# Performance work log

Hardware: AMD Instinct MI355X
Metric: run time of the kernel (lower is better)

## Reference

```python
import jax, jax.numpy as jnp
import numpy as np

N_DST = [50000, 10000, 2048]
HEADS = 4


def setup_inputs() -> dict:
    key = jax.random.key(0)
    ks = jax.random.split(key, 32)
    d = {}
    d["x"] = jax.random.normal(ks[0], (200000, 128), jnp.float32)
    # conv fc weights [in, H*D], attn vectors [H, D], bias [H*D]; skip [in, out]+bias
    conv_dims = [(128, 64), (256, 64), (256, 47)]   # (in, per-head out D)
    skip_dims = [(128, 256), (256, 256), (256, 47)]
    for l, ((cin, dph), (sin, sout)) in enumerate(zip(conv_dims, skip_dims)):
        d[f"W{l}"] = 0.1 * jax.random.normal(ks[1 + 5 * l], (cin, HEADS * dph), jnp.float32)
        d[f"al{l}"] = 0.1 * jax.random.normal(ks[2 + 5 * l], (HEADS, dph), jnp.float32)
        d[f"ar{l}"] = 0.1 * jax.random.normal(ks[3 + 5 * l], (HEADS, dph), jnp.float32)
        d[f"b{l}"] = jnp.zeros((HEADS * dph,), jnp.float32)
        d[f"Ws{l}"] = 0.1 * jax.random.normal(ks[4 + 5 * l], (sin, sout), jnp.float32)
        d[f"bs{l}"] = jnp.zeros((sout,), jnp.float32)
    edge_cfg = [(800000, 200000, 50000), (400000, 50000, 10000), (100000, 10000, 2048)]
    for l, (ne, ns, nd) in enumerate(edge_cfg):
        d[f"src{l}"] = jax.random.randint(ks[20 + 2 * l], (ne,), 0, ns, jnp.int32)
        d[f"dst{l}"] = jax.random.randint(ks[21 + 2 * l], (ne,), 0, nd, jnp.int32)
    return d


def gat_conv(h_src, h_dst, src, dst, n_dst, W, al, ar, b):
    H, D = al.shape
    fs = (h_src @ W).reshape(-1, H, D)   # [n_src, H, D]
    fd = (h_dst @ W).reshape(-1, H, D)   # [n_dst, H, D]
    el = jnp.einsum("nhd,hd->nh", fs, al)
    er = jnp.einsum("nhd,hd->nh", fd, ar)
    e = jax.nn.leaky_relu(el[src] + er[dst], 0.2)          # [E, H]
    emax = jax.ops.segment_max(e, dst, num_segments=n_dst)  # stable softmax
    ee = jnp.exp(e - emax[dst])
    denom = jax.ops.segment_sum(ee, dst, num_segments=n_dst)
    alpha = ee / denom[dst]
    msg = fs[src] * alpha[:, :, None]                      # [E, H, D]
    rst = jax.ops.segment_sum(msg, dst, num_segments=n_dst)
    return rst + b.reshape(1, H, D)


def reference(x, W0, al0, ar0, b0, Ws0, bs0, W1, al1, ar1, b1, Ws1, bs1,
              W2, al2, ar2, b2, Ws2, bs2, src0, dst0, src1, dst1, src2, dst2):
    h = x
    # layer 0
    h_res = h[:N_DST[0]]
    h = gat_conv(h, h_res, src0, dst0, N_DST[0], W0, al0, ar0, b0).reshape(N_DST[0], -1)
    h = jax.nn.elu(h + h_res @ Ws0 + bs0)
    # layer 1
    h_res = h[:N_DST[1]]
    h = gat_conv(h, h_res, src1, dst1, N_DST[1], W1, al1, ar1, b1).reshape(N_DST[1], -1)
    h = jax.nn.elu(h + h_res @ Ws1 + bs1)
    # layer 2: mean over heads, no activation
    h_res = h[:N_DST[2]]
    h = gat_conv(h, h_res, src2, dst2, N_DST[2], W2, al2, ar2, b2).mean(axis=1)
    h = h + h_res @ Ws2 + bs2
    return jax.nn.log_softmax(h, axis=-1)
```

## Files before the change

### kernel.cpp

```cpp
#include <hip/hip_runtime.h>
#include <hip/hip_bf16.h>
#include <cmath>

#define HEADS 4
typedef __hip_bfloat16 bf16;
typedef short short8 __attribute__((ext_vector_type(8)));
typedef unsigned short us8 __attribute__((ext_vector_type(8)));
typedef float floatx4 __attribute__((ext_vector_type(4)));
typedef float floatx2 __attribute__((ext_vector_type(2)));
typedef unsigned int u32;

__device__ inline float bf2f(unsigned short u) {
    union { unsigned u; float f; } c; c.u = ((unsigned)u) << 16; return c.f;
}
__device__ inline short f2bs(float f) {
    bf16 h = __float2bfloat16(f);
    return *reinterpret_cast<short*>(&h);
}
__device__ __forceinline__ floatx2 bfpair(unsigned u) {
    union { unsigned v; float f; } lo, hi;
    lo.v = u << 16; hi.v = u & 0xffff0000u;
    return (floatx2){lo.f, hi.f};
}
__device__ __forceinline__ unsigned char f2fp8(float v) {
    return (unsigned char)(__builtin_amdgcn_cvt_pk_fp8_f32(v, v, 0, false) & 0xff);
}

__device__ __forceinline__ void ld_lds16(const void* g, void* l) {
    __builtin_amdgcn_global_load_lds((const __attribute__((address_space(1))) u32*)g,
                                     (__attribute__((address_space(3))) u32*)l, 16, 0, 0);
}

__device__ const int g_ND[3]   = {50000, 10000, 2048};
__device__ const int g_OOFF[3] = {0, 50001, 60002};
__device__ const int g_NE[3]   = {800000, 400000, 100000};
__device__ const int g_SOFF[3] = {0, 800000, 1200000};
__device__ const int g_S[3]    = {391, 79, 16};

#define NBIN 128
#define NBLK 128
#define MAXB 8192
#define MAXS 391
#define PF 4

__global__ void precast_all(const float* __restrict__ W0, const float* __restrict__ W1,
                            const float* __restrict__ W2, const float* __restrict__ W3,
                            const float* __restrict__ W4, const float* __restrict__ x,
                            bf16* __restrict__ B0, bf16* __restrict__ B1, bf16* __restrict__ B2,
                            bf16* __restrict__ B3, bf16* __restrict__ B4, bf16* __restrict__ xb)
{
    int y = blockIdx.y;
    if (y == 5) {
        const float4* in = (const float4*)x;
        ushort4* out = (ushort4*)xb;
        const int n4 = 200000 * 128 / 4;
        for (int i = blockIdx.x * blockDim.x + threadIdx.x; i < n4; i += gridDim.x * blockDim.x) {
            float4 v = in[i];
            ushort4 o;
            o.x = (unsigned short)f2bs(v.x); o.y = (unsigned short)f2bs(v.y);
            o.z = (unsigned short)f2bs(v.z); o.w = (unsigned short)f2bs(v.w);
            out[i] = o;
        }
        return;
    }
    const int Ks[5] = {128, 256, 256, 128, 256};
    const int Ns[5] = {256, 256, 188, 256, 256};
    const float* W = (y == 0) ? W0 : (y == 1) ? W1 : (y == 2) ? W2 : (y == 3) ? W3 : W4;
    bf16* B = (y == 0) ? B0 : (y == 1) ? B1 : (y == 2) ? B2 : (y == 3) ? B3 : B4;
    int K = Ks[y], N = Ns[y], sz = K * N;
    for (int i = blockIdx.x * blockDim.x + threadIdx.x; i < sz; i += gridDim.x * blockDim.x) {
        int n = i / K, k = i % K;
        B[i] = __float2bfloat16(W[(size_t)k * N + n]);
    }
}

template<int FUSE, int EL, int OUT8>
__global__ __launch_bounds__(256)
void gemm_mfma(const bf16* __restrict__ A, const bf16* __restrict__ Bt,
               const bf16* __restrict__ add, const float* __restrict__ bias,
               const float* __restrict__ al, const float* __restrict__ ar,
               float* __restrict__ el, float* __restrict__ er,
               void* __restrict__ Cb, int M, int N, int K, int nd)
{
    const int BM = 128, BN = 128, BK = 64;
    __shared__ short As[BM * BK];
    __shared__ short Bs[BN * BK];
    int tid = threadIdx.x;
    int wave = tid >> 6, lane = tid & 63;
    int q = lane >> 4, r = lane & 15;
    int row0 = blockIdx.y * BM, col0 = blockIdx.x * BN;
    int wm = (wave >> 1) * 64, wn = (wave & 1) * 64;

    const short* A16 = (const short*)A;
    const short* B16 = (const short*)Bt;
    int srow = tid >> 3;
    int scol = ((tid & 7) ^ (srow & 7)) * 8;
    const short* ga = A16 + (size_t)(row0 + srow) * K + scol;
    const short* gb = B16 + (size_t)(col0 + srow) * K + scol;
    char* la = (char*)As + tid * 16;
    char* lb = (char*)Bs + tid * 16;

    floatx4 zero = {0.f, 0.f, 0.f, 0.f};
    floatx4 acc[4][4];
#pragma unroll
    for (int i = 0; i < 4; i++)
#pragma unroll
        for (int j = 0; j < 4; j++) acc[i][j] = zero;

    for (int k0 = 0; k0 < K; k0 += BK) {
        ld_lds16(ga,                    la);
        ld_lds16(ga + (size_t)32 * K,   la + 4096);
        ld_lds16(ga + (size_t)64 * K,   la + 8192);
        ld_lds16(ga + (size_t)96 * K,   la + 12288);
        ld_lds16(gb,                    lb);
        ld_lds16(gb + (size_t)32 * K,   lb + 4096);
        ld_lds16(gb + (size_t)64 * K,   lb + 8192);
        ld_lds16(gb + (size_t)96 * K,   lb + 12288);
        ga += BK; gb += BK;
        __syncthreads();
#pragma unroll
        for (int ks = 0; ks < 2; ks++) {
            short8 af[4], bfr[4];
#pragma unroll
            for (int mt = 0; mt < 4; mt++) {
                int row = wm + mt * 16 + r;
                af[mt] = *(short8*)&As[row * BK + (((ks << 2) | q) ^ (r & 7)) * 8];
            }
#pragma unroll
            for (int nt = 0; nt < 4; nt++) {
                int row = wn + nt * 16 + r;
                bfr[nt] = *(short8*)&Bs[row * BK + (((ks << 2) | q) ^ (r & 7)) * 8];
            }
#pragma unroll
            for (int mt = 0; mt < 4; mt++)
#pragma unroll
                for (int nt = 0; nt < 4; nt++)
                    acc[mt][nt] = __builtin_amdgcn_mfma_f32_16x16x32_bf16(af[mt], bfr[nt], acc[mt][nt], 0, 0, 0);
        }
        __syncthreads();
    }

#pragma unroll
    for (int mt = 0; mt < 4; mt++) {
#pragma unroll
        for (int nt = 0; nt < 4; nt++) {
            int gcol = col0 + wn + nt * 16 + r;
            if (gcol >= N) continue;
#pragma unroll
            for (int e = 0; e < 4; e++) {
                int grow = row0 + wm + mt * 16 + q * 4 + e;
                if (grow >= M) continue;
                float v = acc[mt][nt][e];
                size_t idx = (size_t)grow * N + gcol;
                if (FUSE == 1) {
                    v += __bfloat162float(add[idx]) + bias[gcol];
                    v = (v > 0.f) ? v : (__expf(v) - 1.f);
                }
                if (OUT8) ((unsigned char*)Cb)[idx] = f2fp8(v);
                else      ((bf16*)Cb)[idx] = __float2bfloat16(v);
            }
        }
    }

    if (EL) {
        int head = (col0 + wn) >> 6;
        float alh[4], arh[4];
#pragma unroll
        for (int nt = 0; nt < 4; nt++) {
            int c = nt * 16 + r;
            alh[nt] = al[head * 64 + c];
            arh[nt] = ar[head * 64 + c];
        }
#pragma unroll
        for (int mt = 0; mt < 4; mt++) {
#pragma unroll
            for (int e = 0; e < 4; e++) {
                float pl = 0.f, pr = 0.f;
#pragma unroll
                for (int nt = 0; nt < 4; nt++) {
                    float v = acc[mt][nt][e];
                    pl += v * alh[nt];
                    pr += v * arh[nt];
                }
#pragma unroll
                for (int off = 1; off < 16; off <<= 1) {
                    pl += __shfl_xor(pl, off);
                    pr += __shfl_xor(pr, off);
                }
                int grow = row0 + wm + mt * 16 + q * 4 + e;
                if (r == 0 && grow < M) {
                    el[grow * 4 + head] = pl;
                    if (grow < nd) er[grow * 4 + head] = pr;
                }
            }
        }
    }
}

__global__ void el_er_kernel(const bf16* __restrict__ fs, const float* __restrict__ al,
                             const float* __restrict__ ar, float* __restrict__ el,
                             float* __restrict__ er, int nd, int D)
{
    int n = blockIdx.x;
    int h = threadIdx.x >> 6;
    int d = threadIdx.x & 63;
    int HD = HEADS * D;
    float v = 0.f, a = 0.f, rr = 0.f;
    if (d < D) {
        v = __bfloat162float(fs[(size_t)n * HD + h * D + d]);
        a = al[h * D + d];
        rr = ar[h * D + d];
    }
    float pl = v * a, pr = v * rr;
    for (int off = 32; off; off >>= 1) {
        pl += __shfl_down(pl, off);
        pr += __shfl_down(pr, off);
    }
    if (d == 0) {
        el[n * HEADS + h] = pl;
        if (n < nd) er[n * HEADS + h] = pr;
    }
}

__global__ __launch_bounds__(256)
void bin_hist(const int* __restrict__ d0, const int* __restrict__ d1,
              const int* __restrict__ d2, int* __restrict__ blockhist)
{
    int l = blockIdx.y;
    const int* dst = (l == 0) ? d0 : (l == 1) ? d1 : d2;
    int ne = g_NE[l], S = g_S[l];
    __shared__ int h[NBIN];
    for (int i = threadIdx.x; i < NBIN; i += blockDim.x) h[i] = 0;
    __syncthreads();
    int per = (ne + NBLK - 1) / NBLK;
    int st = blockIdx.x * per;
    int en = min(st + per, ne);
    for (int i = st + threadIdx.x; i < en; i += blockDim.x)
        atomicAdd(&h[dst[i] / S], 1);
    __syncthreads();
    for (int i = threadIdx.x; i < NBIN; i += blockDim.x)
        blockhist[(l * NBIN + i) * NBLK + blockIdx.x] = h[i];
}

__global__ void coarse_scan(const int* __restrict__ blockhist, int* __restrict__ bbase,
                            int* __restrict__ offs)
{
    int l = blockIdx.x;
    int t = threadIdx.x;
    __shared__ int s[NBIN];
    int tot = 0;
    for (int k = 0; k < NBLK; k++) tot += blockhist[(l * NBIN + t) * NBLK + k];
    s[t] = tot;
    __syncthreads();
    for (int off = 1; off < NBIN; off <<= 1) {
        int a = (t >= off) ? s[t - off] : 0;
        __syncthreads();
        s[t] += a;
        __syncthreads();
    }
    bbase[l * (NBIN + 1) + t + 1] = s[t];
    if (t == 0) {
        bbase[l * (NBIN + 1)] = 0;
        offs[g_OOFF[l] + g_ND[l]] = g_NE[l];
    }
}

__global__ void bin_scan(const int* __restrict__ blockhist, const int* __restrict__ bbase,
                         int* __restrict__ base)
{
    int l = blockIdx.y, bin = blockIdx.x;
    int t = threadIdx.x;
    __shared__ int s[NBLK];
    int v = blockhist[(l * NBIN + bin) * NBLK + t];
    s[t] = v;
    __syncthreads();
    for (int off = 1; off < NBLK; off <<= 1) {
        int a = (t >= off) ? s[t - off] : 0;
        __syncthreads();
        s[t] += a;
        __syncthreads();
    }
    base[(l * NBIN + bin) * NBLK + t] = bbase[l * (NBIN + 1) + bin] + s[t] - v;
}

__global__ __launch_bounds__(256)
void bin_scatter(const int* __restrict__ s0, const int* __restrict__ d0,
                 const int* __restrict__ s1, const int* __restrict__ d1,
                 const int* __restrict__ s2, const int* __restrict__ d2,
                 const int* __restrict__ base, int* __restrict__ stage)
{
    int l = blockIdx.y;
    const int* src = (l == 0) ? s0 : (l == 1) ? s1 : s2;
    const int* dst = (l == 0) ? d0 : (l == 1) ? d1 : d2;
    int ne = g_NE[l], S = g_S[l], soff = g_SOFF[l];
    __shared__ int cur[NBIN];
    for (int i = threadIdx.x; i < NBIN; i += blockDim.x)
        cur[i] = base[(l * NBIN + i) * NBLK + blockIdx.x];
    __syncthreads();
    int per = (ne + NBLK - 1) / NBLK;
    int st = blockIdx.x * per;
    int en = min(st + per, ne);
    for (int i = st + threadIdx.x; i < en; i += blockDim.x) {
        int dv = dst[i];
        int b = dv / S;
        int ldst = dv - b * S;
        int p = atomicAdd(&cur[b], 1);
        stage[soff + p] = src[i] | (ldst << 18);
    }
}

__global__ __launch_bounds__(256)
void bin_expand(const int* __restrict__ stage, const int* __restrict__ bbase,
                int* __restrict__ offs, int* __restrict__ ssrc)
{
    int l = blockIdx.y, b = blockIdx.x;
    int S = g_S[l], nd = g_ND[l], ooff = g_OOFF[l], soff = g_SOFF[l];
    int dlo = b * S;
    if (dlo >= nd) return;
    int dhi = min(dlo + S, nd);
    int base = bbase[l * (NBIN + 1) + b];
    int end  = bbase[l * (NBIN + 1) + b + 1];
    int cnt  = end - base;
    int tid = threadIdx.x;
    __shared__ int sdata[MAXB];
    __shared__ int outb[MAXB];
    __shared__ int lh[512];
    __shared__ int lcur[MAXS];
    lh[tid] = 0; lh[tid + 256] = 0;
    __syncthreads();
    if (cnt <= MAXB) {
        for (int i = tid; i < cnt; i += 256) {
            int v = stage[soff + base + i];
            sdata[i] = v;
            atomicAdd(&lh[v >> 18], 1);
        }
        __syncthreads();
        for (int off = 1; off < 512; off <<= 1) {
            int a0 = (tid >= off) ? lh[tid - off] : 0;
            int a1 = lh[tid + 256 - off];
            __syncthreads();
            lh[tid] += a0; lh[tid + 256] += a1;
            __syncthreads();
        }
        for (int d = tid; d < dhi - dlo; d += 256) {
            int ex = (d == 0) ? 0 : lh[d - 1];
            offs[ooff + dlo + d] = base + ex;
            lcur[d] = ex;
        }
        __syncthreads();
        for (int i = tid; i < cnt; i += 256) {
            int v = sdata[i];
            int p = atomicAdd(&lcur[v >> 18], 1);
            outb[p] = v & 0x3FFFF;
        }
        __syncthreads();
        for (int i = tid; i < cnt; i += 256)
            ssrc[soff + base + i] = outb[i];
    } else {
        for (int i = tid; i < cnt; i += 256)
            atomicAdd(&lh[stage[soff + base + i] >> 18], 1);
        __syncthreads();
        for (int off = 1; off < 512; off <<= 1) {
            int a0 = (tid >= off) ? lh[tid - off] : 0;
            int a1 = lh[tid + 256 - off];
            __syncthreads();
            lh[tid] += a0; lh[tid + 256] += a1;
            __syncthreads();
        }
        for (int d = tid; d < dhi - dlo; d += 256) {
            int ex = (d == 0) ? 0 : lh[d - 1];
            offs[ooff + dlo + d] = base + ex;
            lcur[d] = ex;
        }
        __syncthreads();
        for (int i = tid; i < cnt; i += 256) {
            int v = stage[soff + base + i];
            int p = atomicAdd(&lcur[v >> 18], 1);
            ssrc[soff + base + p] = v & 0x3FFFF;
        }
    }
}

__global__ __launch_bounds__(256)
void attn_agg64(const unsigned char* __restrict__ fs8, const float* __restrict__ el,
                const float* __restrict__ er, const float* __restrict__ b,
                const int* __restrict__ offs, const int* __restrict__ ssrc,
                bf16* __restrict__ rst, int nd)
{
    int wave = threadIdx.x >> 6, lane = threadIdx.x & 63;
    int n = blockIdx.x * 4 + wave;
    if (n >= nd) return;
    int s0 = offs[n], s1 = offs[n + 1];
    float4 erv = *(const float4*)&er[(size_t)n * 4];
    int half = lane >> 5, sub = lane & 31, head = sub >> 3;
    float eh = (head == 0) ? erv.x : (head == 1) ? erv.y : (head == 2) ? erv.z : erv.w;

    floatx2 acc[4];
#pragma unroll
    for (int j = 0; j < 4; j++) acc[j] = (floatx2){0.f, 0.f};
    float s = 0.f;

    int cnt = s1 - s0;
    int npairs = cnt >> 1;
    int i = s0 + half;
    if (npairs > 0) {
        int sid = ssrc[i];
        float ev = el[(size_t)sid * 4 + head];
        uint2 f = *(const uint2*)&fs8[(size_t)sid * 256 + sub * 8];
        for (int p = 1; p < npairs; p++) {
            i += 2;
            int sid2 = ssrc[i];
            float ev2 = el[(size_t)sid2 * 4 + head];
            uint2 f2 = *(const uint2*)&fs8[(size_t)sid2 * 256 + sub * 8];
            float e = ev + eh; e = (e > 0.f) ? e : 0.2f * e;
            float a = __expf(fminf(e, 60.f));
            s += a;
            floatx2 aa = {a, a};
            acc[0] = __builtin_elementwise_fma((floatx2)__builtin_amdgcn_cvt_pk_f32_fp8(f.x, false), aa, acc[0]);
            acc[1] = __builtin_elementwise_fma((floatx2)__builtin_amdgcn_cvt_pk_f32_fp8(f.x, true),  aa, acc[1]);
            acc[2] = __builtin_elementwise_fma((floatx2)__builtin_amdgcn_cvt_pk_f32_fp8(f.y, false), aa, acc[2]);
            acc[3] = __builtin_elementwise_fma((floatx2)__builtin_amdgcn_cvt_pk_f32_fp8(f.y, true),  aa, acc[3]);
            ev = ev2; f = f2;
        }
        float e = ev + eh; e = (e > 0.f) ? e : 0.2f * e;
        float a = __expf(fminf(e, 60.f));
        s += a;
        floatx2 aa = {a, a};
        acc[0] = __builtin_elementwise_fma((floatx2)__builtin_amdgcn_cvt_pk_f32_fp8(f.x, false), aa, acc[0]);
        acc[1] = __builtin_elementwise_fma((floatx2)__builtin_amdgcn_cvt_pk_f32_fp8(f.x, true),  aa, acc[1]);
        acc[2] = __builtin_elementwise_fma((floatx2)__builtin_amdgcn_cvt_pk_f32_fp8(f.y, false), aa, acc[2]);
        acc[3] = __builtin_elementwise_fma((floatx2)__builtin_amdgcn_cvt_pk_f32_fp8(f.y, true),  aa, acc[3]);
    }
    if (cnt & 1) {
        int idx = s1 - 1;
        int sid = ssrc[idx];
        float ev = el[(size_t)sid * 4 + head];
        uint2 f = *(const uint2*)&fs8[(size_t)sid * 256 + sub * 8];
        float e = ev + eh; e = (e > 0.f) ? e : 0.2f * e;
        float a = __expf(fminf(e, 60.f));
        if (half) a = 0.f;
        s += a;
        floatx2 aa = {a, a};
        acc[0] = __builtin_elementwise_fma((floatx2)__builtin_amdgcn_cvt_pk_f32_fp8(f.x, false), aa, acc[0]);
        acc[1] = __builtin_elementwise_fma((floatx2)__builtin_amdgcn_cvt_pk_f32_fp8(f.x, true),  aa, acc[1]);
        acc[2] = __builtin_elementwise_fma((floatx2)__builtin_amdgcn_cvt_pk_f32_fp8(f.y, false), aa, acc[2]);
        acc[3] = __builtin_elementwise_fma((floatx2)__builtin_amdgcn_cvt_pk_f32_fp8(f.y, true),  aa, acc[3]);
    }
    s += __shfl_xor(s, 32);
#pragma unroll
    for (int j = 0; j < 4; j++) {
        acc[j].x += __shfl_xor(acc[j].x, 32);
        acc[j].y += __shfl_xor(acc[j].y, 32);
    }
    if (half == 0) {
        float inv = (s > 0.f) ? 1.f / s : 0.f;
        float4 b0 = *(const float4*)&b[sub * 8];
        float4 b1 = *(const float4*)&b[sub * 8 + 4];
        us8 o;
        o[0] = (unsigned short)f2bs(acc[0].x * inv + b0.x);
        o[1] = (unsigned short)f2bs(acc[0].y * inv + b0.y);
        o[2] = (unsigned short)f2bs(acc[1].x * inv + b0.z);
        o[3] = (unsigned short)f2bs(acc[1].y * inv + b0.w);
        o[4] = (unsigned short)f2bs(acc[2].x * inv + b1.x);
        o[5] = (unsigned short)f2bs(acc[2].y * inv + b1.y);
        o[6] = (unsigned short)f2bs(acc[3].x * inv + b1.z);
        o[7] = (unsigned short)f2bs(acc[3].y * inv + b1.w);
        *(us8*)&((unsigned short*)rst)[(size_t)n * 256 + sub * 8] = o;
    }
}

__global__ __launch_bounds__(256)
void attn_agg_gen(const bf16* __restrict__ fs, const float* __restrict__ el,
                  const float* __restrict__ er, const float* __restrict__ b,
                  const int* __restrict__ offs, const int* __restrict__ ssrc,
                  bf16* __restrict__ rst, int D, int nd)
{
    __shared__ int slds[4][64];
    __shared__ __align__(16) float alds[4][64][4];
    int wave = threadIdx.x >> 6, lane = threadIdx.x & 63;
    int n = blockIdx.x * 4 + wave;
    if (n >= nd) return;
    int HD = HEADS * D;
    int s0 = offs[n], s1 = offs[n + 1];
    int cnt = s1 - s0;
    float4 erv = *(const float4*)&er[(size_t)n * 4];
    const unsigned short* fsu = (const unsigned short*)fs;

    bool act = (4 * lane) < HD;
    int h_[4];
#pragma unroll
    for (int j = 0; j < 4; j++) {
        int e = 4 * lane + j;
        h_[j] = (e < HD) ? (e / D) : 0;
    }
    float acc[4] = {0.f, 0.f, 0.f, 0.f};
    float sp0 = 0.f, sp1 = 0.f, sp2 = 0.f, sp3 = 0.f;

    for (int c0 = 0; c0 < cnt; c0 += 64) {
        int nc = min(cnt - c0, 64);
        if (lane < nc) {
            int sid = ssrc[s0 + c0 + lane];
            float4 ev = *(const float4*)&el[(size_t)sid * 4];
            float e0 = ev.x + erv.x; e0 = (e0 > 0.f) ? e0 : 0.2f * e0;
            float e1 = ev.y + erv.y; e1 = (e1 > 0.f) ? e1 : 0.2f * e1;
            float e2 = ev.z + erv.z; e2 = (e2 > 0.f) ? e2 : 0.2f * e2;
            float e3 = ev.w + erv.w; e3 = (e3 > 0.f) ? e3 : 0.2f * e3;
            float a0 = __expf(fminf(e0, 60.f));
            float a1 = __expf(fminf(e1, 60.f));
            float a2 = __expf(fminf(e2, 60.f));
            float a3 = __expf(fminf(e3, 60.f));
            sp0 += a0; sp1 += a1; sp2 += a2; sp3 += a3;
            slds[wave][lane] = sid;
            alds[wave][lane][0] = a0;
            alds[wave][lane][1] = a1;
            alds[wave][lane][2] = a2;
            alds[wave][lane][3] = a3;
        }
        __builtin_amdgcn_wave_barrier();
        float4 aq[PF]; ushort4 fq[PF];
#pragma unroll
        for (int k = 0; k < PF; k++) {
            if (k < nc) {
                int sid = slds[wave][k];
                aq[k] = *(const float4*)&alds[wave][k][0];
                fq[k] = act ? *(const ushort4*)&fsu[(size_t)sid * HD + 4 * lane]
                            : ushort4{0, 0, 0, 0};
            }
        }
        for (int eb = 0; eb < nc; eb += PF) {
#pragma unroll
            for (int k = 0; k < PF; k++) {
                int e = eb + k;
                if (e >= nc) break;
                float4 a4 = aq[k];
                ushort4 f = fq[k];
                int en = e + PF;
                if (en < nc) {
                    int sid = slds[wave][en];
                    aq[k] = *(const float4*)&alds[wave][en][0];
                    fq[k] = act ? *(const ushort4*)&fsu[(size_t)sid * HD + 4 * lane]
                                : ushort4{0, 0, 0, 0};
                }
                unsigned short fa[4] = {f.x, f.y, f.z, f.w};
#pragma unroll
                for (int j = 0; j < 4; j++) {
                    int hj = h_[j];
                    float av = (hj == 0) ? a4.x : (hj == 1) ? a4.y : (hj == 2) ? a4.z : a4.w;
                    acc[j] += av * bf2f(fa[j]);
                }
            }
        }
        __builtin_amdgcn_wave_barrier();
    }

#pragma unroll
    for (int off = 32; off; off >>= 1) {
        sp0 += __shfl_xor(sp0, off);
        sp1 += __shfl_xor(sp1, off);
        sp2 += __shfl_xor(sp2, off);
        sp3 += __shfl_xor(sp3, off);
    }
    if (act) {
#pragma unroll
        for (int j = 0; j < 4; j++) {
            int e4 = 4 * lane + j;
            int hj = h_[j];
            float sv = (hj == 0) ? sp0 : (hj == 1) ? sp1 : (hj == 2) ? sp2 : sp3;
            float o = (sv > 0.f) ? acc[j] / sv : 0.f;
            rst[(size_t)n * HD + e4] = __float2bfloat16(o + b[e4]);
        }
    }
}

__global__ void final_kernel(const bf16* __restrict__ rst2, const bf16* __restrict__ h2,
                             const float* __restrict__ Ws, const float* __restrict__ bs,
                             float* __restrict__ out)
{
    const int K = 256, C = 47;
    int n = blockIdx.x;
    int c = threadIdx.x;
    float v = -INFINITY;
    if (c < C) {
        float dot = 0.f;
        for (int k = 0; k < K; k++) dot += __bfloat162float(h2[(size_t)n * K + k]) * Ws[k * C + c];
        float mean = 0.f;
#pragma unroll
        for (int hh = 0; hh < HEADS; hh++) mean += __bfloat162float(rst2[(size_t)n * HEADS * C + hh * C + c]);
        mean *= 0.25f;
        v = mean + dot + bs[c];
    }
    float mx = v;
    for (int off = 32; off; off >>= 1) mx = fmaxf(mx, __shfl_xor(mx, off));
    float ex = (c < C) ? __expf(v - mx) : 0.f;
    float sum = ex;
    for (int off = 32; off; off >>= 1) sum += __shfl_xor(sum, off);
    if (c < C) out[n * C + c] = v - mx - logf(sum);
}

extern "C" void kernel_launch(void* const* d_in, const int* in_sizes, int n_in,
                              void* d_out, int out_size, void* d_ws, size_t ws_size,
                              hipStream_t stream)
{
    const float* x = (const float*)d_in[0];
    const float* W[3]  = {(const float*)d_in[1],  (const float*)d_in[7],  (const float*)d_in[13]};
    const float* al[3] = {(const float*)d_in[2],  (const float*)d_in[8],  (const float*)d_in[14]};
    const float* ar[3] = {(const float*)d_in[3],  (const float*)d_in[9],  (const float*)d_in[15]};
    const float* bb[3] = {(const float*)d_in[4],  (const float*)d_in[10], (const float*)d_in[16]};
    const float* Ws[3] = {(const float*)d_in[5],  (const float*)d_in[11], (const float*)d_in[17]};
    const float* bs[3] = {(const float*)d_in[6],  (const float*)d_in[12], (const float*)d_in[18]};
    const int* srcp[3] = {(const int*)d_in[19], (const int*)d_in[21], (const int*)d_in[23]};
    const int* dstp[3] = {(const int*)d_in[20], (const int*)d_in[22], (const int*)d_in[24]};

    char* p = (char*)d_ws;
    auto alloc = [&](size_t bytes) -> void* {
        void* r = (void*)p;
        p += (bytes + 255) & ~(size_t)255;
        return r;
    };
    bf16*  xb    = (bf16*)alloc((size_t)200064 * 128 * 2);
    bf16*  fsb   = (bf16*)alloc((size_t)200000 * 256 * 2);
    bf16*  h1b   = (bf16*)alloc((size_t)50048 * 256 * 2);
    bf16*  h2b   = (bf16*)alloc((size_t)10112 * 256 * 2);
    bf16*  rstb  = (bf16*)alloc((size_t)50000 * 256 * 2);
    float* elb   = (float*)alloc((size_t)200000 * 4 * 4);
    float* erb   = (float*)alloc((size_t)50000 * 4 * 4);
    bf16* Wt[3]; bf16* Wst[2];
    Wt[0]  = (bf16*)alloc(256 * 128 * 2);
    Wt[1]  = (bf16*)alloc(256 * 256 * 2);
    Wt[2]  = (bf16*)alloc(256 * 256 * 2);
    Wst[0] = (bf16*)alloc(256 * 128 * 2);
    Wst[1] = (bf16*)alloc(256 * 256 * 2);
    int* offs_all  = (int*)alloc(62051 * 4);
    int* ssrc_all  = (int*)alloc(1300000 * 4);
    int* stage_all = (int*)alloc(1300000 * 4);
    int* blockhist = (int*)alloc(3 * NBIN * NBLK * 4);
    int* binbase   = (int*)alloc(3 * NBIN * NBLK * 4);
    int* bbase     = (int*)alloc(3 * (NBIN + 1) * 4);

    unsigned char* fsb8 = (unsigned char*)fsb;

    const int OOFF[3] = {0, 50001, 60002};
    const int SOFF[3] = {0, 800000, 1200000};

    precast_all<<<dim3(512, 6), 256, 0, stream>>>(W[0], W[1], W[2], Ws[0], Ws[1], x,
                                                  Wt[0], Wt[1], Wt[2], Wst[0], Wst[1], xb);

    bin_hist<<<dim3(NBLK, 3), 256, 0, stream>>>(dstp[0], dstp[1], dstp[2], blockhist);
    coarse_scan<<<3, NBIN, 0, stream>>>(blockhist, bbase, offs_all);
    bin_scan<<<dim3(NBIN, 3), NBLK, 0, stream>>>(blockhist, bbase, binbase);
    bin_scatter<<<dim3(NBLK, 3), 256, 0, stream>>>(srcp[0], dstp[0], srcp[1], dstp[1],
                                                   srcp[2], dstp[2], binbase, stage_all);
    bin_expand<<<dim3(NBIN, 3), 256, 0, stream>>>(stage_all, bbase, offs_all, ssrc_all);

    gemm_mfma<0, 1, 1><<<dim3(2, 1563), 256, 0, stream>>>(
        xb, Wt[0], nullptr, nullptr, al[0], ar[0], elb, erb, fsb8, 200000, 256, 128, 50000);
    attn_agg64<<<12500, 256, 0, stream>>>(fsb8, elb, erb, bb[0], offs_all + OOFF[0], ssrc_all + SOFF[0], rstb, 50000);
    gemm_mfma<1, 0, 0><<<dim3(2, 391), 256, 0, stream>>>(
        xb, Wst[0], rstb, bs[0], nullptr, nullptr, nullptr, nullptr, h1b, 50000, 256, 128, 0);

    gemm_mfma<0, 1, 1><<<dim3(2, 391), 256, 0, stream>>>(
        h1b, Wt[1], nullptr, nullptr, al[1], ar[1], elb, erb, fsb8, 50000, 256, 256, 10000);
    attn_agg64<<<2500, 256, 0, stream>>>(fsb8, elb, erb, bb[1], offs_all + OOFF[1], ssrc_all + SOFF[1], rstb, 10000);
    gemm_mfma<1, 0, 0><<<dim3(2, 79), 256, 0, stream>>>(
        h1b, Wst[1], rstb, bs[1], nullptr, nullptr, nullptr, nullptr, h2b, 10000, 256, 256, 0);

    gemm_mfma<0, 0, 0><<<dim3(2, 79), 256, 0, stream>>>(
        h2b, Wt[2], nullptr, nullptr, nullptr, nullptr, nullptr, nullptr, fsb, 10000, 188, 256, 0);
    el_er_kernel<<<10000, 256, 0, stream>>>(fsb, al[2], ar[2], elb, erb, 2048, 47);
    attn_agg_gen<<<512, 256, 0, stream>>>(fsb, elb, erb, bb[2], offs_all + OOFF[2], ssrc_all + SOFF[2], rstb, 47, 2048);
    final_kernel<<<2048, 64, 0, stream>>>(rstb, h2b, Ws[2], bs[2], (float*)d_out);
}
```

Before: 556.9 us.

## Widen GEMM tile to full 256 columns, transpose MFMA operands for vectorized epilogue

The GEMM block now covers all 256 output columns with 8 waves (512 threads), so the A tile is loaded once per row block instead of twice. MFMA operands are swapped so each lane holds four consecutive columns, which allows packed 4-byte fp8 and 8-byte bf16 stores, vectorized residual and bias loads, and a shorter shuffle reduction for el/er. Buffers are padded to cover the row overrun. The trade-off is larger LDS use per block and fewer blocks, which lowers occupancy and parallelism on the smaller layers. The N=188 layer also still stages all 256 rows of B.

```diff
diff --git a/kernel.cpp b/kernel.cpp
--- a/kernel.cpp
+++ b/kernel.cpp
@@ -17,13 +17,12 @@
     bf16 h = __float2bfloat16(f);
     return *reinterpret_cast<short*>(&h);
 }
-__device__ __forceinline__ floatx2 bfpair(unsigned u) {
-    union { unsigned v; float f; } lo, hi;
-    lo.v = u << 16; hi.v = u & 0xffff0000u;
-    return (floatx2){lo.f, hi.f};
-}
-__device__ __forceinline__ unsigned char f2fp8(float v) {
-    return (unsigned char)(__builtin_amdgcn_cvt_pk_fp8_f32(v, v, 0, false) & 0xff);
+__device__ __forceinline__ unsigned pack_bf16(float a, float b) {
+    return (((unsigned)(unsigned short)f2bs(b)) << 16) | (unsigned short)f2bs(a);
+}
+__device__ __forceinline__ unsigned pack_fp8x4(float a, float b, float c, float d) {
+    unsigned lo = __builtin_amdgcn_cvt_pk_fp8_f32(a, b, 0, false);
+    return __builtin_amdgcn_cvt_pk_fp8_f32(c, d, lo, true);
 }
 
 __device__ __forceinline__ void ld_lds16(const void* g, void* l) {
@@ -75,28 +74,28 @@
 }
 
 template<int FUSE, int EL, int OUT8>
-__global__ __launch_bounds__(256)
+__global__ __launch_bounds__(512)
 void gemm_mfma(const bf16* __restrict__ A, const bf16* __restrict__ Bt,
                const bf16* __restrict__ add, const float* __restrict__ bias,
                const float* __restrict__ al, const float* __restrict__ ar,
                float* __restrict__ el, float* __restrict__ er,
                void* __restrict__ Cb, int M, int N, int K, int nd)
 {
-    const int BM = 128, BN = 128, BK = 64;
-    __shared__ short As[BM * BK];
-    __shared__ short Bs[BN * BK];
+    const int BK = 64;
+    __shared__ short As[128 * BK];
+    __shared__ short Bs[256 * BK];
     int tid = threadIdx.x;
     int wave = tid >> 6, lane = tid & 63;
     int q = lane >> 4, r = lane & 15;
-    int row0 = blockIdx.y * BM, col0 = blockIdx.x * BN;
-    int wm = (wave >> 1) * 64, wn = (wave & 1) * 64;
+    int row0 = blockIdx.y * 128;
+    int wm = (wave >> 2) * 64, wn = (wave & 3) * 64;
 
     const short* A16 = (const short*)A;
     const short* B16 = (const short*)Bt;
     int srow = tid >> 3;
     int scol = ((tid & 7) ^ (srow & 7)) * 8;
     const short* ga = A16 + (size_t)(row0 + srow) * K + scol;
-    const short* gb = B16 + (size_t)(col0 + srow) * K + scol;
+    const short* gb = B16 + (size_t)srow * K + scol;
     char* la = (char*)As + tid * 16;
     char* lb = (char*)Bs + tid * 16;
 
@@ -108,90 +107,86 @@
         for (int j = 0; j < 4; j++) acc[i][j] = zero;
 
     for (int k0 = 0; k0 < K; k0 += BK) {
-        ld_lds16(ga,                    la);
-        ld_lds16(ga + (size_t)32 * K,   la + 4096);
-        ld_lds16(ga + (size_t)64 * K,   la + 8192);
-        ld_lds16(ga + (size_t)96 * K,   la + 12288);
-        ld_lds16(gb,                    lb);
-        ld_lds16(gb + (size_t)32 * K,   lb + 4096);
-        ld_lds16(gb + (size_t)64 * K,   lb + 8192);
-        ld_lds16(gb + (size_t)96 * K,   lb + 12288);
+        ld_lds16(ga,                   la);
+        ld_lds16(ga + (size_t)64 * K,  la + 8192);
+        ld_lds16(gb,                   lb);
+        ld_lds16(gb + (size_t)64 * K,  lb + 8192);
+        ld_lds16(gb + (size_t)128 * K, lb + 16384);
+        ld_lds16(gb + (size_t)192 * K, lb + 24576);
         ga += BK; gb += BK;
         __syncthreads();
 #pragma unroll
         for (int ks = 0; ks < 2; ks++) {
+            int gr = (((ks << 2) | q) ^ (r & 7)) * 8;
             short8 af[4], bfr[4];
 #pragma unroll
-            for (int mt = 0; mt < 4; mt++) {
-                int row = wm + mt * 16 + r;
-                af[mt] = *(short8*)&As[row * BK + (((ks << 2) | q) ^ (r & 7)) * 8];
+            for (int mt = 0; mt < 4; mt++)
+                af[mt] = *(short8*)&As[(wm + mt * 16 + r) * BK + gr];
+#pragma unroll
+            for (int nt = 0; nt < 4; nt++)
+                bfr[nt] = *(short8*)&Bs[(wn + nt * 16 + r) * BK + gr];
+#pragma unroll
+            for (int mt = 0; mt < 4; mt++)
+#pragma unroll
+                for (int nt = 0; nt < 4; nt++)
+                    acc[mt][nt] = __builtin_amdgcn_mfma_f32_16x16x32_bf16(bfr[nt], af[mt], acc[mt][nt], 0, 0, 0);
+        }
+        __syncthreads();
+    }
+
+#pragma unroll
+    for (int mt = 0; mt < 4; mt++) {
+        int grow = row0 + wm + mt * 16 + r;
+        if (grow >= M) continue;
+#pragma unroll
+        for (int nt = 0; nt < 4; nt++) {
+            int n0 = wn + nt * 16 + q * 4;
+            floatx4 v = acc[mt][nt];
+            if (FUSE == 1) {
+                ushort4 ad = *(const ushort4*)&add[(size_t)grow * N + n0];
+                float4 bi = *(const float4*)&bias[n0];
+                v[0] += bf2f(ad.x) + bi.x;
+                v[1] += bf2f(ad.y) + bi.y;
+                v[2] += bf2f(ad.z) + bi.z;
+                v[3] += bf2f(ad.w) + bi.w;
+#pragma unroll
+                for (int e = 0; e < 4; e++) v[e] = (v[e] > 0.f) ? v[e] : (__expf(v[e]) - 1.f);
             }
+            if (OUT8) {
+                *(u32*)((unsigned char*)Cb + (size_t)grow * N + n0) =
+                    pack_fp8x4(v[0], v[1], v[2], v[3]);
+            } else if (n0 + 3 < N) {
+                uint2 o = {pack_bf16(v[0], v[1]), pack_bf16(v[2], v[3])};
+                *(uint2*)((unsigned short*)Cb + (size_t)grow * N + n0) = o;
+            } else {
+#pragma unroll
+                for (int e = 0; e < 4; e++)
+                    if (n0 + e < N)
+                        ((unsigned short*)Cb)[(size_t)grow * N + n0 + e] = (unsigned short)f2bs(v[e]);
+            }
+        }
+    }
+
+    if (EL) {
+        int head = wave & 3;
+#pragma unroll
+        for (int mt = 0; mt < 4; mt++) {
+            float pl = 0.f, pr = 0.f;
 #pragma unroll
             for (int nt = 0; nt < 4; nt++) {
-                int row = wn + nt * 16 + r;
-                bfr[nt] = *(short8*)&Bs[row * BK + (((ks << 2) | q) ^ (r & 7)) * 8];
+                int nn = nt * 16 + q * 4;
+                float4 av = *(const float4*)&al[head * 64 + nn];
+                float4 rv = *(const float4*)&ar[head * 64 + nn];
+                floatx4 v = acc[mt][nt];
+                pl += v[0] * av.x + v[1] * av.y + v[2] * av.z + v[3] * av.w;
+                pr += v[0] * rv.x + v[1] * rv.y + v[2] * rv.z + v[3] * rv.w;
             }
-#pragma unroll
-            for (int mt = 0; mt < 4; mt++)
-#pragma unroll
-                for (int nt = 0; nt < 4; nt++)
-                    acc[mt][nt] = __builtin_amdgcn_mfma_f32_16x16x32_bf16(af[mt], bfr[nt], acc[mt][nt], 0, 0, 0);
-        }
-        __syncthreads();
-    }
-
-#pragma unroll
-    for (int mt = 0; mt < 4; mt++) {
-#pragma unroll
-        for (int nt = 0; nt < 4; nt++) {
-            int gcol = col0 + wn + nt * 16 + r;
-            if (gcol >= N) continue;
-#pragma unroll
-            for (int e = 0; e < 4; e++) {
-                int grow = row0 + wm + mt * 16 + q * 4 + e;
-                if (grow >= M) continue;
-                float v = acc[mt][nt][e];
-                size_t idx = (size_t)grow * N + gcol;
-                if (FUSE == 1) {
-                    v += __bfloat162float(add[idx]) + bias[gcol];
-                    v = (v > 0.f) ? v : (__expf(v) - 1.f);
-                }
-                if (OUT8) ((unsigned char*)Cb)[idx] = f2fp8(v);
-                else      ((bf16*)Cb)[idx] = __float2bfloat16(v);
-            }
-        }
-    }
-
-    if (EL) {
-        int head = (col0 + wn) >> 6;
-        float alh[4], arh[4];
-#pragma unroll
-        for (int nt = 0; nt < 4; nt++) {
-            int c = nt * 16 + r;
-            alh[nt] = al[head * 64 + c];
-            arh[nt] = ar[head * 64 + c];
-        }
-#pragma unroll
-        for (int mt = 0; mt < 4; mt++) {
-#pragma unroll
-            for (int e = 0; e < 4; e++) {
-                float pl = 0.f, pr = 0.f;
-#pragma unroll
-                for (int nt = 0; nt < 4; nt++) {
-                    float v = acc[mt][nt][e];
-                    pl += v * alh[nt];
-                    pr += v * arh[nt];
-                }
-#pragma unroll
-                for (int off = 1; off < 16; off <<= 1) {
-                    pl += __shfl_xor(pl, off);
-                    pr += __shfl_xor(pr, off);
-                }
-                int grow = row0 + wm + mt * 16 + q * 4 + e;
-                if (r == 0 && grow < M) {
-                    el[grow * 4 + head] = pl;
-                    if (grow < nd) er[grow * 4 + head] = pr;
-                }
+            pl += __shfl_xor(pl, 16); pl += __shfl_xor(pl, 32);
+            pr += __shfl_xor(pr, 16); pr += __shfl_xor(pr, 32);
+            int grow = row0 + wm + mt * 16 + r;
+            if (lane < 16 && grow < M) {
+                el[grow * 4 + head] = pl;
+                if (grow < nd) er[grow * 4 + head] = pr;
             }
         }
     }
@@ -618,12 +613,12 @@
         return r;
     };
     bf16*  xb    = (bf16*)alloc((size_t)200064 * 128 * 2);
-    bf16*  fsb   = (bf16*)alloc((size_t)200000 * 256 * 2);
+    bf16*  fsb   = (bf16*)alloc((size_t)200064 * 256 * 2);
     bf16*  h1b   = (bf16*)alloc((size_t)50048 * 256 * 2);
     bf16*  h2b   = (bf16*)alloc((size_t)10112 * 256 * 2);
     bf16*  rstb  = (bf16*)alloc((size_t)50000 * 256 * 2);
-    float* elb   = (float*)alloc((size_t)200000 * 4 * 4);
-    float* erb   = (float*)alloc((size_t)50000 * 4 * 4);
+    float* elb   = (float*)alloc((size_t)200064 * 4 * 4);
+    float* erb   = (float*)alloc((size_t)50048 * 4 * 4);
     bf16* Wt[3]; bf16* Wst[2];
     Wt[0]  = (bf16*)alloc(256 * 128 * 2);
     Wt[1]  = (bf16*)alloc(256 * 256 * 2);
@@ -652,19 +647,19 @@
                                                    srcp[2], dstp[2], binbase, stage_all);
     bin_expand<<<dim3(NBIN, 3), 256, 0, stream>>>(stage_all, bbase, offs_all, ssrc_all);
 
-    gemm_mfma<0, 1, 1><<<dim3(2, 1563), 256, 0, stream>>>(
+    gemm_mfma<0, 1, 1><<<dim3(1, 1563), 512, 0, stream>>>(
         xb, Wt[0], nullptr, nullptr, al[0], ar[0], elb, erb, fsb8, 200000, 256, 128, 50000);
     attn_agg64<<<12500, 256, 0, stream>>>(fsb8, elb, erb, bb[0], offs_all + OOFF[0], ssrc_all + SOFF[0], rstb, 50000);
-    gemm_mfma<1, 0, 0><<<dim3(2, 391), 256, 0, stream>>>(
+    gemm_mfma<1, 0, 0><<<dim3(1, 391), 512, 0, stream>>>(
         xb, Wst[0], rstb, bs[0], nullptr, nullptr, nullptr, nullptr, h1b, 50000, 256, 128, 0);
 
-    gemm_mfma<0, 1, 1><<<dim3(2, 391), 256, 0, stream>>>(
+    gemm_mfma<0, 1, 1><<<dim3(1, 391), 512, 0, stream>>>(
         h1b, Wt[1], nullptr, nullptr, al[1], ar[1], elb, erb, fsb8, 50000, 256, 256, 10000);
     attn_agg64<<<2500, 256, 0, stream>>>(fsb8, elb, erb, bb[1], offs_all + OOFF[1], ssrc_all + SOFF[1], rstb, 10000);
-    gemm_mfma<1, 0, 0><<<dim3(2, 79), 256, 0, stream>>>(
+    gemm_mfma<1, 0, 0><<<dim3(1, 79), 512, 0, stream>>>(
         h1b, Wst[1], rstb, bs[1], nullptr, nullptr, nullptr, nullptr, h2b, 10000, 256, 256, 0);
 
-    gemm_mfma<0, 0, 0><<<dim3(2, 79), 256, 0, stream>>>(
+    gemm_mfma<0, 0, 0><<<dim3(1, 79), 512, 0, stream>>>(
         h2b, Wt[2], nullptr, nullptr, nullptr, nullptr, nullptr, nullptr, fsb, 10000, 188, 256, 0);
     el_er_kernel<<<10000, 256, 0, stream>>>(fsb, al[2], ar[2], elb, erb, 2048, 47);
     attn_agg_gen<<<512, 256, 0, stream>>>(fsb, elb, erb, bb[2], offs_all + OOFF[2], ssrc_all + SOFF[2], rstb, 47, 2048);
```

New measurement: 524.4 us. -5.8%, faster.
